# Kernel tuning notes

Hardware: AMD Instinct MI355X
Metric: run time of the kernel (lower is better)

The kernel has to match this reference:

```python
import jax, jax.numpy as jnp
import numpy as np

N = 80000       # nodes
E = 1280000     # edges (avg degree 16)
G = 2000        # graphs
NSHAPE, NCOLOR, POSMAX = 16, 16, 1024
HID, OUT, IN_DIM = 64, 2, 40
EPS = 1e-5


def setup_inputs() -> dict:
    key = jax.random.key(0)
    ks = jax.random.split(key, 20)
    f32 = jnp.float32
    return {
        "shape_id": jax.random.randint(ks[0], (N,), 0, NSHAPE),
        "color_id": jax.random.randint(ks[1], (N,), 0, NCOLOR),
        "pos_id": jax.random.randint(ks[2], (N,), 0, POSMAX),
        "edge_index": jax.random.randint(ks[3], (2, E), 0, N),
        "batch": jnp.sort(jax.random.randint(ks[4], (N,), 0, G)),
        "num_graphs": G,
        "shape_tab": jax.random.normal(ks[5], (NSHAPE, 16), f32),
        "color_tab": jax.random.normal(ks[6], (NCOLOR, 16), f32),
        "pos_tab": jax.random.normal(ks[7], (POSMAX, 8), f32),
        "W1l": jax.random.normal(ks[8], (IN_DIM, HID), f32) / np.sqrt(IN_DIM),
        "b1": jnp.zeros((HID,), f32),
        "W1r": jax.random.normal(ks[9], (IN_DIM, HID), f32) / np.sqrt(IN_DIM),
        "g1": jnp.ones((HID,), f32),
        "be1": jnp.zeros((HID,), f32),
        "W2l": jax.random.normal(ks[10], (HID, HID), f32) / np.sqrt(HID),
        "b2": jnp.zeros((HID,), f32),
        "W2r": jax.random.normal(ks[11], (HID, HID), f32) / np.sqrt(HID),
        "g2": jnp.ones((HID,), f32),
        "be2": jnp.zeros((HID,), f32),
        "Wout": jax.random.normal(ks[12], (HID, OUT), f32) / np.sqrt(HID),
        "bout": jnp.zeros((OUT,), f32),
    }


def sage_conv(x, src, dst, Wl, b, Wr, n_nodes):
    # PyG SAGEConv (mean aggr): out = lin_l(mean_{j in N(i)} x_j) + lin_r(x_i)
    agg = jax.ops.segment_sum(x[src], dst, num_segments=n_nodes)     # [N, F]
    deg = jax.ops.segment_sum(jnp.ones((src.shape[0], 1), x.dtype), dst,
                              num_segments=n_nodes)                  # [N, 1]
    agg = agg / jnp.maximum(deg, 1.0)
    return agg @ Wl + b + x @ Wr


def batch_norm(x, gamma, beta):
    # training-mode BatchNorm1d over nodes
    m = x.mean(axis=0)
    v = x.var(axis=0)
    return (x - m) * (gamma / jnp.sqrt(v + EPS)) + beta


def reference(shape_id, color_id, pos_id, edge_index, batch, num_graphs,
              shape_tab, color_tab, pos_tab,
              W1l, b1, W1r, g1, be1,
              W2l, b2, W2r, g2, be2,
              Wout, bout):
    n_nodes = shape_id.shape[0]
    src, dst = edge_index[0], edge_index[1]
    x = jnp.concatenate([shape_tab[shape_id], color_tab[color_id],
                         pos_tab[pos_id]], axis=-1)                  # [N, 40]
    x = jax.nn.relu(batch_norm(sage_conv(x, src, dst, W1l, b1, W1r, n_nodes), g1, be1))
    # dropout: eval mode -> identity
    x = jax.nn.relu(batch_norm(sage_conv(x, src, dst, W2l, b2, W2r, n_nodes), g2, be2))
    # global mean pool over batch segments
    summed = jax.ops.segment_sum(x, batch, num_segments=num_graphs)   # [G, H]
    counts = jax.ops.segment_sum(jnp.ones((n_nodes, 1), x.dtype), batch,
                                 num_segments=num_graphs)
    pooled = summed / jnp.maximum(counts, 1.0)
    return pooled @ Wout + bout                                       # [G, 2]
```

## Files before the change

### kernel.cpp

```cpp
#include <hip/hip_runtime.h>

#define NN 80000
#define NE 1280000
#define NG 2000
#define HID 64
#define FIN1 40
#define BSZ 128
#define NBUK (NN / BSZ)
#define EB 8192
#define NBB ((NE + EB - 1) / EB)
#define NBBP 160
constexpr float EPS = 1e-5f;

typedef _Float16 f16;
typedef f16 f16x8 __attribute__((ext_vector_type(8)));
typedef float f32x4 __attribute__((ext_vector_type(4)));

__global__ void setup(const int* __restrict__ sid, const int* __restrict__ cid,
                      const int* __restrict__ pid, const int* __restrict__ batch,
                      const float* __restrict__ stab, const float* __restrict__ ctab,
                      const float* __restrict__ ptab,
                      const float* __restrict__ W1l, const float* __restrict__ W1r,
                      const float* __restrict__ W2l, const float* __restrict__ W2r,
                      int* __restrict__ ids, f16* __restrict__ Bt1, f16* __restrict__ Bt2,
                      int* __restrict__ gstart,
                      f16* __restrict__ stab16, f16* __restrict__ ctab16,
                      f16* __restrict__ ptab16) {
    int bid = blockIdx.x;
    int tid = threadIdx.x;
    if (bid < 313) {
        int n = bid * 256 + tid;
        if (n < NN) ids[n] = sid[n] | (cid[n] << 4) | (pid[n] << 8);
    } else if (bid < 373) {
        int i = (bid - 313) * 256 + tid;
        if (i < 64 * 104) {
            int j = i / 104, k = i - j * 104;
            float v = 0.f;
            if (k < 40) v = W1l[k * 64 + j];
            else if (k < 80) v = W1r[(k - 40) * 64 + j];
            Bt1[i] = (f16)v;
        }
        int i2 = i - 64 * 104;
        if (i2 >= 0 && i2 < 64 * 136) {
            int j = i2 / 136, k = i2 - j * 136;
            float v = 0.f;
            if (k < 64) v = W2l[k * 64 + j];
            else if (k < 128) v = W2r[(k - 64) * 64 + j];
            Bt2[i2] = (f16)v;
        }
    } else if (bid < 686) {
        int n = (bid - 373) * 256 + tid;
        if (n >= NN) return;
        int cur = batch[n];
        int prev = (n == 0) ? -1 : batch[n - 1];
        for (int g = prev + 1; g <= cur; g++) gstart[g] = n;
        if (n == NN - 1)
            for (int g = cur + 1; g <= NG; g++) gstart[g] = NN;
    } else {
        int i = (bid - 686) * 256 + tid;
        if (i < 256) stab16[i] = (f16)stab[i];
        else if (i < 512) ctab16[i - 256] = (f16)ctab[i - 256];
        else if (i < 512 + 8192) ptab16[i - 512] = (f16)ptab[i - 512];
    }
}

__global__ void khist(const int* __restrict__ dst, int* __restrict__ bhistT,
                      int* __restrict__ bcnt) {
    __shared__ int lh[NBUK];
    for (int i = threadIdx.x; i < NBUK; i += 256) lh[i] = 0;
    __syncthreads();
    int e0 = blockIdx.x * EB, e1 = min(e0 + EB, NE);
    for (int e = e0 + threadIdx.x; e < e1; e += 256) atomicAdd(&lh[dst[e] >> 7], 1);
    __syncthreads();
    for (int i = threadIdx.x; i < NBUK; i += 256) {
        int c = lh[i];
        bhistT[i * NBBP + blockIdx.x] = c;
        if (c) atomicAdd(&bcnt[i], c);
    }
}

__global__ void kscan_a(const int* __restrict__ bcnt, int* __restrict__ bstart) {
    __shared__ int l[1024];
    int t = threadIdx.x;
    l[t] = (t < NBUK) ? bcnt[t] : 0;
    __syncthreads();
    for (int off = 1; off < 1024; off <<= 1) {
        int v = (t >= off) ? l[t - off] : 0;
        __syncthreads();
        l[t] += v;
        __syncthreads();
    }
    if (t < NBUK) bstart[t] = (t == 0) ? 0 : l[t - 1];
    if (t == NBUK) bstart[NBUK] = NE;
}

__global__ void kscan_b(const int* __restrict__ bhistT, const int* __restrict__ bstart,
                        int* __restrict__ lbaseT) {
    int b = blockIdx.x;
    int l = threadIdx.x;
    int run = bstart[b];
    for (int i0 = 0; i0 < NBB; i0 += 64) {
        int idx = i0 + l;
        int v = (idx < NBB) ? bhistT[b * NBBP + idx] : 0;
        int inc = v;
        for (int off = 1; off < 64; off <<= 1) {
            int tt = __shfl_up(inc, off);
            if (l >= off) inc += tt;
        }
        if (idx < NBB) lbaseT[b * NBBP + idx] = run + inc - v;
        run += __shfl(inc, 63);
    }
}

__global__ void kbin(const int* __restrict__ src, const int* __restrict__ dst,
                     const int* __restrict__ lbaseT, int* __restrict__ ebuf) {
    __shared__ int lcur[NBUK];
    for (int i = threadIdx.x; i < NBUK; i += 256) lcur[i] = lbaseT[i * NBBP + blockIdx.x];
    __syncthreads();
    int e0 = blockIdx.x * EB, e1 = min(e0 + EB, NE);
    for (int e = e0 + threadIdx.x; e < e1; e += 256) {
        int d = dst[e];
        int off = atomicAdd(&lcur[d >> 7], 1);
        ebuf[off] = (src[e] << 7) | (d & 127);
    }
}

__global__ void kfill(const int* __restrict__ ebuf, const int* __restrict__ bstart,
                      int* __restrict__ row_ptr, int* __restrict__ eidx) {
    __shared__ int cnt[BSZ];
    __shared__ int sb[BSZ];
    __shared__ int lcur[BSZ];
    int b = blockIdx.x, t = threadIdx.x;
    int nbase = b << 7;
    if (t < BSZ) cnt[t] = 0;
    __syncthreads();
    int s0 = bstart[b], s1 = bstart[b + 1];
    for (int i = s0 + t; i < s1; i += 256) atomicAdd(&cnt[ebuf[i] & 127], 1);
    __syncthreads();
    if (t < BSZ) sb[t] = cnt[t];
    __syncthreads();
    for (int off = 1; off < BSZ; off <<= 1) {
        int v = (t >= off && t < BSZ) ? sb[t - off] : 0;
        __syncthreads();
        if (t < BSZ) sb[t] += v;
        __syncthreads();
    }
    if (t < BSZ) {
        int excl = ((t == 0) ? 0 : sb[t - 1]) + s0;
        row_ptr[nbase + t] = excl;
        lcur[t] = excl;
    }
    if (b == 0 && t == 0) row_ptr[NN] = NE;
    __syncthreads();
    for (int i = s0 + t; i < s1; i += 256) {
        int v = ebuf[i];
        int pos = atomicAdd(&lcur[v & 127], 1);
        eidx[pos] = v >> 7;
    }
}

__global__ void gather1(const int* __restrict__ row_ptr, const int* __restrict__ eidx,
                        const int* __restrict__ ids,
                        const f16* __restrict__ stab16, const f16* __restrict__ ctab16,
                        const f16* __restrict__ ptab16, f16* __restrict__ agg) {
    int tt = blockIdx.x * 256 + threadIdx.x;
    int n = tt >> 6;
    int lane = threadIdx.x & 63;
    if (n >= NN) return;
    int grp = lane >> 3, li = lane & 7;
    int beg = row_ptr[n], end = row_ptr[n + 1];
    float ac[8];
#pragma unroll
    for (int i = 0; i < 8; i++) ac[i] = 0.f;
    for (int j0 = beg; j0 < end; j0 += 64) {
        int cnt = min(64, end - j0);
        int myid = (j0 + lane < end) ? eidx[j0 + lane] : 0;
        int steps = (cnt + 7) >> 3;
        for (int u = 0; u < steps; u++) {
            int e = u * 8 + grp;
            int s = __shfl(myid, e);
            if (e < cnt && li < 5) {
                int id = ids[s];
                const f16* rowp;
                if (li < 2)      rowp = &stab16[(id & 15) * 16 + li * 8];
                else if (li < 4) rowp = &ctab16[((id >> 4) & 15) * 16 + (li - 2) * 8];
                else             rowp = &ptab16[(id >> 8) * 8];
                f16x8 v = *(const f16x8*)rowp;
#pragma unroll
                for (int i = 0; i < 8; i++) ac[i] += (float)v[i];
            }
        }
    }
#pragma unroll
    for (int m = 8; m <= 32; m <<= 1) {
#pragma unroll
        for (int i = 0; i < 8; i++) ac[i] += __shfl_xor(ac[i], m);
    }
    if (lane < 5) {
        float inv = 1.0f / (float)max(end - beg, 1);
        f16x8 o;
#pragma unroll
        for (int i = 0; i < 8; i++) o[i] = (f16)(ac[i] * inv);
        *(f16x8*)&agg[(size_t)n * FIN1 + lane * 8] = o;
    }
}

__global__ void gather2(const int* __restrict__ row_ptr, const int* __restrict__ eidx,
                        const f16* __restrict__ x, const float* __restrict__ stats,
                        const float* __restrict__ g1, const float* __restrict__ be1,
                        f16* __restrict__ agg) {
    int tt = blockIdx.x * 256 + threadIdx.x;
    int n = tt >> 6;
    int lane = threadIdx.x & 63;
    if (n >= NN) return;
    int grp = lane >> 3;
    int fl = (lane & 7) * 8;
    float sc8[8], sh8[8];
    {
        const float invn = 1.0f / (float)NN;
#pragma unroll
        for (int i = 0; i < 8; i++) {
            float m = stats[fl + i] * invn;
            float var = stats[64 + fl + i] * invn - m * m;
            float sc = g1[fl + i] * __frsqrt_rn(var + EPS);
            sc8[i] = sc;
            sh8[i] = be1[fl + i] - m * sc;
        }
    }
    int beg = row_ptr[n], end = row_ptr[n + 1];
    float ac[8];
#pragma unroll
    for (int i = 0; i < 8; i++) ac[i] = 0.f;
    for (int j0 = beg; j0 < end; j0 += 64) {
        int cnt = min(64, end - j0);
        int myid = (j0 + lane < end) ? eidx[j0 + lane] : 0;
        int steps = (cnt + 7) >> 3;
        for (int u = 0; u < steps; u++) {
            int e = u * 8 + grp;
            int s = __shfl(myid, e);
            if (e < cnt) {
                f16x8 v = *(const f16x8*)&x[(size_t)s * HID + fl];
#pragma unroll
                for (int i = 0; i < 8; i++)
                    ac[i] += fmaxf(fmaf((float)v[i], sc8[i], sh8[i]), 0.f);
            }
        }
    }
#pragma unroll
    for (int m = 8; m <= 32; m <<= 1) {
#pragma unroll
        for (int i = 0; i < 8; i++) ac[i] += __shfl_xor(ac[i], m);
    }
    if (lane < 8) {
        float inv = 1.0f / (float)max(end - beg, 1);
        f16x8 o;
#pragma unroll
        for (int i = 0; i < 8; i++) o[i] = (f16)(ac[i] * inv);
        *(f16x8*)&agg[(size_t)n * HID + fl] = o;
    }
}

__launch_bounds__(256)
__global__ void sage_mfma1(const int* __restrict__ ids, const f16* __restrict__ aggv,
                           const f16* __restrict__ stab16, const f16* __restrict__ ctab16,
                           const f16* __restrict__ ptab16,
                           const f16* __restrict__ Btg, const float* __restrict__ bias,
                           f16* __restrict__ h, float* __restrict__ stats) {
    __shared__ float sred[4][64];
    __shared__ float qred[4][64];
    const int KP = 104;

    int tid = threadIdx.x;
    int n0 = blockIdx.x * 64;
    int w = tid >> 6, l = tid & 63;
    int jloc = l & 15, kg = l >> 4;
    int n = n0 + w * 16 + jloc;

    f16x8 af[3];
#pragma unroll
    for (int kk = 0; kk < 3; kk++) {
        int c = kk * 4 + kg;
        if (c < 5) {
            af[kk] = *(const f16x8*)&aggv[(size_t)n * FIN1 + c * 8];
        } else if (c < 10) {
            int id = ids[n];
            int cc = c - 5;
            const f16* rowp;
            if (cc < 2)      rowp = &stab16[(id & 15) * 16 + cc * 8];
            else if (cc < 4) rowp = &ctab16[((id >> 4) & 15) * 16 + (cc - 2) * 8];
            else             rowp = &ptab16[(id >> 8) * 8];
            af[kk] = *(const f16x8*)rowp;
        } else {
#pragma unroll
            for (int i = 0; i < 8; i++) af[kk][i] = (f16)0.f;
        }
    }

    f32x4 acc[4];
#pragma unroll
    for (int jt = 0; jt < 4; jt++) {
        float bj = bias[jt * 16 + jloc];
        acc[jt] = (f32x4){bj, bj, bj, bj};
    }
#pragma unroll
    for (int kk = 0; kk < 3; kk++) {
#pragma unroll
        for (int jt = 0; jt < 4; jt++) {
            f16x8 bf = *(const f16x8*)&Btg[(jt * 16 + jloc) * KP + kk * 32 + kg * 8];
            acc[jt] = __builtin_amdgcn_mfma_f32_16x16x32_f16(af[kk], bf, acc[jt], 0, 0, 0);
        }
    }
#pragma unroll
    for (int jt = 0; jt < 4; jt++) {
        float sv = 0.f, qv = 0.f;
#pragma unroll
        for (int reg = 0; reg < 4; reg++) {
            f16 hv = (f16)acc[jt][reg];
            int nn2 = n0 + w * 16 + kg * 4 + reg;
            h[(size_t)nn2 * HID + jt * 16 + jloc] = hv;
            float v = (float)hv;
            sv += v; qv += v * v;
        }
        sv += __shfl_xor(sv, 16); sv += __shfl_xor(sv, 32);
        qv += __shfl_xor(qv, 16); qv += __shfl_xor(qv, 32);
        if (kg == 0) { sred[w][jt * 16 + jloc] = sv; qred[w][jt * 16 + jloc] = qv; }
    }
    __syncthreads();
    if (tid < 128) {
        int f2 = tid & 63, which = tid >> 6;
        float r = which ? (qred[0][f2] + qred[1][f2] + qred[2][f2] + qred[3][f2])
                        : (sred[0][f2] + sred[1][f2] + sred[2][f2] + sred[3][f2]);
        atomicAdd(&stats[which * 64 + f2], r);
    }
}

__launch_bounds__(256)
__global__ void sage_mfma2(const f16* __restrict__ x, const f16* __restrict__ aggv,
                           const f16* __restrict__ Btg, const float* __restrict__ bias,
                           f16* __restrict__ h,
                           const float* __restrict__ stats1, const float* __restrict__ g1,
                           const float* __restrict__ be1, float* __restrict__ stats) {
    __shared__ float ssc[64], ssh[64];
    __shared__ float sred[4][64];
    __shared__ float qred[4][64];
    const int KP = 136;

    int tid = threadIdx.x;
    int n0 = blockIdx.x * 64;
    if (tid < 64) {
        const float invn = 1.0f / (float)NN;
        float m = stats1[tid] * invn;
        float var = stats1[64 + tid] * invn - m * m;
        float sc = g1[tid] * __frsqrt_rn(var + EPS);
        ssc[tid] = sc;
        ssh[tid] = be1[tid] - m * sc;
    }
    __syncthreads();

    int w = tid >> 6, l = tid & 63;
    int jloc = l & 15, kg = l >> 4;
    int n = n0 + w * 16 + jloc;

    f16x8 af[4];
#pragma unroll
    for (int kk = 0; kk < 4; kk++) {
        int c = kk * 4 + kg;
        if (c < 8) {
            af[kk] = *(const f16x8*)&aggv[(size_t)n * HID + c * 8];
        } else {
            int fb = (c - 8) * 8;
            f16x8 vx = *(const f16x8*)&x[(size_t)n * HID + fb];
#pragma unroll
            for (int i = 0; i < 8; i++)
                af[kk][i] = (f16)fmaxf(fmaf((float)vx[i], ssc[fb + i], ssh[fb + i]), 0.f);
        }
    }

    f32x4 acc[4];
#pragma unroll
    for (int jt = 0; jt < 4; jt++) {
        float bj = bias[jt * 16 + jloc];
        acc[jt] = (f32x4){bj, bj, bj, bj};
    }
#pragma unroll
    for (int kk = 0; kk < 4; kk++) {
#pragma unroll
        for (int jt = 0; jt < 4; jt++) {
            f16x8 bf = *(const f16x8*)&Btg[(jt * 16 + jloc) * KP + kk * 32 + kg * 8];
            acc[jt] = __builtin_amdgcn_mfma_f32_16x16x32_f16(af[kk], bf, acc[jt], 0, 0, 0);
        }
    }
#pragma unroll
    for (int jt = 0; jt < 4; jt++) {
        float sv = 0.f, qv = 0.f;
#pragma unroll
        for (int reg = 0; reg < 4; reg++) {
            f16 hv = (f16)acc[jt][reg];
            int nn2 = n0 + w * 16 + kg * 4 + reg;
            h[(size_t)nn2 * HID + jt * 16 + jloc] = hv;
            float v = (float)hv;
            sv += v; qv += v * v;
        }
        sv += __shfl_xor(sv, 16); sv += __shfl_xor(sv, 32);
        qv += __shfl_xor(qv, 16); qv += __shfl_xor(qv, 32);
        if (kg == 0) { sred[w][jt * 16 + jloc] = sv; qred[w][jt * 16 + jloc] = qv; }
    }
    __syncthreads();
    if (tid < 128) {
        int f2 = tid & 63, which = tid >> 6;
        float r = which ? (qred[0][f2] + qred[1][f2] + qred[2][f2] + qred[3][f2])
                        : (sred[0][f2] + sred[1][f2] + sred[2][f2] + sred[3][f2]);
        atomicAdd(&stats[which * 64 + f2], r);
    }
}

__global__ void pool_out(const f16* __restrict__ h, const float* __restrict__ stats2,
                         const float* __restrict__ g2, const float* __restrict__ be2,
                         const int* __restrict__ gstart,
                         const float* __restrict__ Wout, const float* __restrict__ bout,
                         float* __restrict__ out) {
    int w = (blockIdx.x * blockDim.x + threadIdx.x) >> 6;
    int f = threadIdx.x & 63;
    if (w >= NG) return;
    const float invn = 1.0f / (float)NN;
    float m = stats2[f] * invn;
    float var = stats2[64 + f] * invn - m * m;
    float sc = g2[f] / sqrtf(var + EPS);
    float sh = be2[f] - m * sc;
    int n0 = gstart[w], n1 = gstart[w + 1];
    float acc = 0.f;
    for (int n = n0; n < n1; n++) {
        float v = fmaf((float)h[(size_t)n * HID + f], sc, sh);
        acc += fmaxf(v, 0.0f);
    }
    float inv = 1.0f / (float)max(n1 - n0, 1);
    float p = acc * inv;
    float a0 = p * Wout[f * 2 + 0];
    float a1 = p * Wout[f * 2 + 1];
#pragma unroll
    for (int mm = 1; mm < 64; mm <<= 1) {
        a0 += __shfl_xor(a0, mm);
        a1 += __shfl_xor(a1, mm);
    }
    if (f == 0) {
        out[w * 2 + 0] = a0 + bout[0];
        out[w * 2 + 1] = a1 + bout[1];
    }
}

extern "C" void kernel_launch(void* const* d_in, const int* in_sizes, int n_in,
                              void* d_out, int out_size, void* d_ws, size_t ws_size,
                              hipStream_t stream) {
    const int* sid = (const int*)d_in[0];
    const int* cid = (const int*)d_in[1];
    const int* pid = (const int*)d_in[2];
    const int* ei = (const int*)d_in[3];
    const int* batch = (const int*)d_in[4];
    const float* stab = (const float*)d_in[6];
    const float* ctab = (const float*)d_in[7];
    const float* ptab = (const float*)d_in[8];
    const float* W1l = (const float*)d_in[9];
    const float* b1 = (const float*)d_in[10];
    const float* W1r = (const float*)d_in[11];
    const float* g1 = (const float*)d_in[12];
    const float* be1 = (const float*)d_in[13];
    const float* W2l = (const float*)d_in[14];
    const float* b2 = (const float*)d_in[15];
    const float* W2r = (const float*)d_in[16];
    const float* g2 = (const float*)d_in[17];
    const float* be2 = (const float*)d_in[18];
    const float* Wout = (const float*)d_in[19];
    const float* bout = (const float*)d_in[20];

    const int* src = ei;
    const int* dst = ei + NE;

    char* p = (char*)d_ws;
    f16* agg = (f16*)p;        p += (size_t)NN * HID * 2;
    f16* h1 = (f16*)p;         p += (size_t)NN * HID * 2;
    f16* h2 = (f16*)p;         p += (size_t)NN * HID * 2;
    f16* bt1 = (f16*)p;        p += 64 * 104 * 2;
    f16* bt2 = (f16*)p;        p += 64 * 136 * 2;
    f16* stab16 = (f16*)p;     p += 256 * 2;
    f16* ctab16 = (f16*)p;     p += 256 * 2;
    f16* ptab16 = (f16*)p;     p += 8192 * 2;
    float* stats = (float*)p;  p += 256 * 4;
    int* bcnt = (int*)p;       p += NBUK * 4;
    int* ids = (int*)p;        p += (size_t)NN * 4;
    int* row_ptr = (int*)p;    p += (NN + 1) * 4;
    int* gstart = (int*)p;     p += (NG + 1) * 4;
    int* bstart = (int*)p;     p += (NBUK + 1) * 4;
    int* bhistT = (int*)p;     p += (size_t)NBUK * NBBP * 4;
    int* lbaseT = (int*)p;     p += (size_t)NBUK * NBBP * 4;
    int* ebuf = (int*)p;       p += (size_t)NE * 4;
    int* eidx = (int*)p;       p += (size_t)NE * 4;

    hipMemsetAsync(stats, 0, 256 * 4 + NBUK * 4, stream);

    const int B = 256;

    setup<<<720, B, 0, stream>>>(sid, cid, pid, batch, stab, ctab, ptab,
                                 W1l, W1r, W2l, W2r,
                                 ids, bt1, bt2, gstart, stab16, ctab16, ptab16);

    khist<<<NBB, B, 0, stream>>>(dst, bhistT, bcnt);
    kscan_a<<<1, 1024, 0, stream>>>(bcnt, bstart);
    kscan_b<<<NBUK, 64, 0, stream>>>(bhistT, bstart, lbaseT);
    kbin<<<NBB, B, 0, stream>>>(src, dst, lbaseT, ebuf);
    kfill<<<NBUK, B, 0, stream>>>(ebuf, bstart, row_ptr, eidx);

    gather1<<<(NN * 64 + B - 1) / B, B, 0, stream>>>(row_ptr, eidx, ids,
                                                     stab16, ctab16, ptab16, agg);
    sage_mfma1<<<NN / 64, B, 0, stream>>>(ids, agg, stab16, ctab16, ptab16,
                                          bt1, b1, h1, stats);

    gather2<<<(NN * 64 + B - 1) / B, B, 0, stream>>>(row_ptr, eidx, h1, stats, g1, be1, agg);
    sage_mfma2<<<NN / 64, B, 0, stream>>>(h1, agg, bt2, b2, h2,
                                          stats, g1, be1, stats + 128);

    pool_out<<<(NG * 64 + B - 1) / B, B, 0, stream>>>(h2, stats + 128, g2, be2, gstart,
                                                      Wout, bout, (float*)d_out);
}
```

Baseline: 234.1 us.

## Repack gather1 lanes 12x5, batch gather loads, fold memset into setup

gather1 now assigns lanes as 12 edge groups times 5 feature slices, so 60 of 64 lanes do useful work where the old 8x8 layout used only 5 of every 8. It issues the eidx, ids and table loads for 5 edges up front to expose memory-level parallelism, and reduces across groups with custom shuffles. gather2 likewise hoists all 8 per-chunk loads before accumulating. The hipMemsetAsync of stats and bcnt is replaced by an extra setup block that zeroes them, which removes one launch. The unrolled loads raise register pressure, and the irregular shuffle reduction adds instructions.

```diff
diff --git a/kernel.cpp b/kernel.cpp
--- a/kernel.cpp
+++ b/kernel.cpp
@@ -25,7 +25,8 @@
                       int* __restrict__ ids, f16* __restrict__ Bt1, f16* __restrict__ Bt2,
                       int* __restrict__ gstart,
                       f16* __restrict__ stab16, f16* __restrict__ ctab16,
-                      f16* __restrict__ ptab16) {
+                      f16* __restrict__ ptab16,
+                      float* __restrict__ stats, int* __restrict__ bcnt) {
     int bid = blockIdx.x;
     int tid = threadIdx.x;
     if (bid < 313) {
@@ -56,11 +57,14 @@
         for (int g = prev + 1; g <= cur; g++) gstart[g] = n;
         if (n == NN - 1)
             for (int g = cur + 1; g <= NG; g++) gstart[g] = NN;
-    } else {
+    } else if (bid < 720) {
         int i = (bid - 686) * 256 + tid;
         if (i < 256) stab16[i] = (f16)stab[i];
         else if (i < 512) ctab16[i - 256] = (f16)ctab[i - 256];
         else if (i < 512 + 8192) ptab16[i - 512] = (f16)ptab[i - 512];
+    } else {
+        if (tid < 256) stats[tid] = 0.f;
+        for (int i = tid; i < NBUK; i += 256) bcnt[i] = 0;
     }
 }
 
@@ -167,34 +171,53 @@
     int n = tt >> 6;
     int lane = threadIdx.x & 63;
     if (n >= NN) return;
-    int grp = lane >> 3, li = lane & 7;
+    int grp = lane / 5;
+    int li = lane - grp * 5;
+    bool lact = grp < 12;
     int beg = row_ptr[n], end = row_ptr[n + 1];
     float ac[8];
 #pragma unroll
     for (int i = 0; i < 8; i++) ac[i] = 0.f;
-    for (int j0 = beg; j0 < end; j0 += 64) {
-        int cnt = min(64, end - j0);
-        int myid = (j0 + lane < end) ? eidx[j0 + lane] : 0;
-        int steps = (cnt + 7) >> 3;
-        for (int u = 0; u < steps; u++) {
-            int e = u * 8 + grp;
-            int s = __shfl(myid, e);
-            if (e < cnt && li < 5) {
-                int id = ids[s];
+    for (int j0 = beg; j0 < end; j0 += 60) {
+        int cnt = min(60, end - j0);
+        bool val[5];
+        int sidx[5];
+#pragma unroll
+        for (int u = 0; u < 5; u++) {
+            int e = u * 12 + grp;
+            val[u] = lact && (e < cnt);
+            sidx[u] = val[u] ? eidx[j0 + e] : 0;
+        }
+        int idv[5];
+#pragma unroll
+        for (int u = 0; u < 5; u++) idv[u] = val[u] ? ids[sidx[u]] : 0;
+        f16x8 v[5];
+#pragma unroll
+        for (int u = 0; u < 5; u++) {
+            if (val[u]) {
+                int id = idv[u];
                 const f16* rowp;
                 if (li < 2)      rowp = &stab16[(id & 15) * 16 + li * 8];
                 else if (li < 4) rowp = &ctab16[((id >> 4) & 15) * 16 + (li - 2) * 8];
                 else             rowp = &ptab16[(id >> 8) * 8];
-                f16x8 v = *(const f16x8*)rowp;
-#pragma unroll
-                for (int i = 0; i < 8; i++) ac[i] += (float)v[i];
+                v[u] = *(const f16x8*)rowp;
             }
         }
-    }
-#pragma unroll
-    for (int m = 8; m <= 32; m <<= 1) {
-#pragma unroll
-        for (int i = 0; i < 8; i++) ac[i] += __shfl_xor(ac[i], m);
+#pragma unroll
+        for (int u = 0; u < 5; u++) {
+            if (val[u]) {
+#pragma unroll
+                for (int i = 0; i < 8; i++) ac[i] += (float)v[u][i];
+            }
+        }
+    }
+#pragma unroll
+    for (int i = 0; i < 8; i++) {
+        float r;
+        r = __shfl(ac[i], lane + 30); if (grp < 6) ac[i] += r;
+        r = __shfl(ac[i], lane + 15); if (grp < 3) ac[i] += r;
+        r = __shfl(ac[i], lane + 10); if (grp < 1) ac[i] += r;
+        r = __shfl(ac[i], lane + 5);  if (grp < 1) ac[i] += r;
     }
     if (lane < 5) {
         float inv = 1.0f / (float)max(end - beg, 1);
@@ -233,16 +256,21 @@
     for (int i = 0; i < 8; i++) ac[i] = 0.f;
     for (int j0 = beg; j0 < end; j0 += 64) {
         int cnt = min(64, end - j0);
-        int myid = (j0 + lane < end) ? eidx[j0 + lane] : 0;
-        int steps = (cnt + 7) >> 3;
-        for (int u = 0; u < steps; u++) {
+        bool val[8];
+        f16x8 v[8];
+#pragma unroll
+        for (int u = 0; u < 8; u++) {
             int e = u * 8 + grp;
-            int s = __shfl(myid, e);
-            if (e < cnt) {
-                f16x8 v = *(const f16x8*)&x[(size_t)s * HID + fl];
+            val[u] = e < cnt;
+            int s = val[u] ? eidx[j0 + e] : 0;
+            if (val[u]) v[u] = *(const f16x8*)&x[(size_t)s * HID + fl];
+        }
+#pragma unroll
+        for (int u = 0; u < 8; u++) {
+            if (val[u]) {
 #pragma unroll
                 for (int i = 0; i < 8; i++)
-                    ac[i] += fmaxf(fmaf((float)v[i], sc8[i], sh8[i]), 0.f);
+                    ac[i] += fmaxf(fmaf((float)v[u][i], sc8[i], sh8[i]), 0.f);
             }
         }
     }
@@ -495,13 +523,12 @@
     int* ebuf = (int*)p;       p += (size_t)NE * 4;
     int* eidx = (int*)p;       p += (size_t)NE * 4;
 
-    hipMemsetAsync(stats, 0, 256 * 4 + NBUK * 4, stream);
-
     const int B = 256;
 
-    setup<<<720, B, 0, stream>>>(sid, cid, pid, batch, stab, ctab, ptab,
+    setup<<<721, B, 0, stream>>>(sid, cid, pid, batch, stab, ctab, ptab,
                                  W1l, W1r, W2l, W2r,
-                                 ids, bt1, bt2, gstart, stab16, ctab16, ptab16);
+                                 ids, bt1, bt2, gstart, stab16, ctab16, ptab16,
+                                 stats, bcnt);
 
     khist<<<NBB, B, 0, stream>>>(dst, bhistT, bcnt);
     kscan_a<<<1, 1024, 0, stream>>>(bcnt, bstart);
```

Result: slower. 250.5 us (+7.0%).

## Hoist layer-1 BN+ReLU into separate pass, accumulate gathers in fp16

Applied to the files above, without the earlier changes.

Adds a bn_apply16 kernel that applies batch-norm and ReLU to h1 once per node in place, so gather2 and sage_mfma2 read normalized values instead of recomputing the affine+ReLU per edge. Both gather kernels now accumulate neighbor features in packed fp16 vectors rather than fp32. The hipMemsetAsync is folded into an extra block of the setup kernel. The changes cut per-edge ALU work and one launch, at the cost of an extra pass over h1 and lower accumulation precision over up to dozens of neighbors.

```diff
diff --git a/kernel.cpp b/kernel.cpp
--- a/kernel.cpp
+++ b/kernel.cpp
@@ -25,7 +25,8 @@
                       int* __restrict__ ids, f16* __restrict__ Bt1, f16* __restrict__ Bt2,
                       int* __restrict__ gstart,
                       f16* __restrict__ stab16, f16* __restrict__ ctab16,
-                      f16* __restrict__ ptab16) {
+                      f16* __restrict__ ptab16,
+                      float* __restrict__ stats, int* __restrict__ bcnt) {
     int bid = blockIdx.x;
     int tid = threadIdx.x;
     if (bid < 313) {
@@ -56,11 +57,14 @@
         for (int g = prev + 1; g <= cur; g++) gstart[g] = n;
         if (n == NN - 1)
             for (int g = cur + 1; g <= NG; g++) gstart[g] = NN;
-    } else {
+    } else if (bid < 720) {
         int i = (bid - 686) * 256 + tid;
         if (i < 256) stab16[i] = (f16)stab[i];
         else if (i < 512) ctab16[i - 256] = (f16)ctab[i - 256];
         else if (i < 512 + 8192) ptab16[i - 512] = (f16)ptab[i - 512];
+    } else {
+        if (tid < 256) stats[tid] = 0.f;
+        for (int i = tid; i < NBUK; i += 256) bcnt[i] = 0;
     }
 }
 
@@ -168,10 +172,11 @@
     int lane = threadIdx.x & 63;
     if (n >= NN) return;
     int grp = lane >> 3, li = lane & 7;
+    bool act = li < 5;
     int beg = row_ptr[n], end = row_ptr[n + 1];
-    float ac[8];
-#pragma unroll
-    for (int i = 0; i < 8; i++) ac[i] = 0.f;
+    f16x8 ach;
+#pragma unroll
+    for (int i = 0; i < 8; i++) ach[i] = (f16)0.f;
     for (int j0 = beg; j0 < end; j0 += 64) {
         int cnt = min(64, end - j0);
         int myid = (j0 + lane < end) ? eidx[j0 + lane] : 0;
@@ -179,18 +184,19 @@
         for (int u = 0; u < steps; u++) {
             int e = u * 8 + grp;
             int s = __shfl(myid, e);
-            if (e < cnt && li < 5) {
+            if (e < cnt && act) {
                 int id = ids[s];
                 const f16* rowp;
                 if (li < 2)      rowp = &stab16[(id & 15) * 16 + li * 8];
                 else if (li < 4) rowp = &ctab16[((id >> 4) & 15) * 16 + (li - 2) * 8];
                 else             rowp = &ptab16[(id >> 8) * 8];
-                f16x8 v = *(const f16x8*)rowp;
-#pragma unroll
-                for (int i = 0; i < 8; i++) ac[i] += (float)v[i];
+                ach += *(const f16x8*)rowp;
             }
         }
     }
+    float ac[8];
+#pragma unroll
+    for (int i = 0; i < 8; i++) ac[i] = (float)ach[i];
 #pragma unroll
     for (int m = 8; m <= 32; m <<= 1) {
 #pragma unroll
@@ -205,32 +211,44 @@
     }
 }
 
+__global__ void bn_apply16(f16* __restrict__ h, const float* __restrict__ stats,
+                           const float* __restrict__ g, const float* __restrict__ be) {
+    __shared__ float ssc[64], ssh[64];
+    int tid = threadIdx.x;
+    if (tid < 64) {
+        const float invn = 1.0f / (float)NN;
+        float m = stats[tid] * invn;
+        float var = stats[64 + tid] * invn - m * m;
+        float sc = g[tid] * __frsqrt_rn(var + EPS);
+        ssc[tid] = sc;
+        ssh[tid] = be[tid] - m * sc;
+    }
+    __syncthreads();
+    int idx = blockIdx.x * 256 + tid;
+    if (idx >= NN * 8) return;
+    int f = (idx & 7) * 8;
+    f16x8 v = *(f16x8*)&h[(size_t)idx * 8];
+    f16x8 o;
+#pragma unroll
+    for (int i = 0; i < 8; i++) {
+        float xv = (float)v[i];
+        o[i] = (f16)fmaxf(fmaf(xv, ssc[f + i], ssh[f + i]), 0.f);
+    }
+    *(f16x8*)&h[(size_t)idx * 8] = o;
+}
+
 __global__ void gather2(const int* __restrict__ row_ptr, const int* __restrict__ eidx,
-                        const f16* __restrict__ x, const float* __restrict__ stats,
-                        const float* __restrict__ g1, const float* __restrict__ be1,
-                        f16* __restrict__ agg) {
+                        const f16* __restrict__ x, f16* __restrict__ agg) {
     int tt = blockIdx.x * 256 + threadIdx.x;
     int n = tt >> 6;
     int lane = threadIdx.x & 63;
     if (n >= NN) return;
     int grp = lane >> 3;
     int fl = (lane & 7) * 8;
-    float sc8[8], sh8[8];
-    {
-        const float invn = 1.0f / (float)NN;
-#pragma unroll
-        for (int i = 0; i < 8; i++) {
-            float m = stats[fl + i] * invn;
-            float var = stats[64 + fl + i] * invn - m * m;
-            float sc = g1[fl + i] * __frsqrt_rn(var + EPS);
-            sc8[i] = sc;
-            sh8[i] = be1[fl + i] - m * sc;
-        }
-    }
     int beg = row_ptr[n], end = row_ptr[n + 1];
-    float ac[8];
-#pragma unroll
-    for (int i = 0; i < 8; i++) ac[i] = 0.f;
+    f16x8 ach;
+#pragma unroll
+    for (int i = 0; i < 8; i++) ach[i] = (f16)0.f;
     for (int j0 = beg; j0 < end; j0 += 64) {
         int cnt = min(64, end - j0);
         int myid = (j0 + lane < end) ? eidx[j0 + lane] : 0;
@@ -239,13 +257,13 @@
             int e = u * 8 + grp;
             int s = __shfl(myid, e);
             if (e < cnt) {
-                f16x8 v = *(const f16x8*)&x[(size_t)s * HID + fl];
-#pragma unroll
-                for (int i = 0; i < 8; i++)
-                    ac[i] += fmaxf(fmaf((float)v[i], sc8[i], sh8[i]), 0.f);
+                ach += *(const f16x8*)&x[(size_t)s * HID + fl];
             }
         }
     }
+    float ac[8];
+#pragma unroll
+    for (int i = 0; i < 8; i++) ac[i] = (float)ach[i];
 #pragma unroll
     for (int m = 8; m <= 32; m <<= 1) {
 #pragma unroll
@@ -337,26 +355,13 @@
 __launch_bounds__(256)
 __global__ void sage_mfma2(const f16* __restrict__ x, const f16* __restrict__ aggv,
                            const f16* __restrict__ Btg, const float* __restrict__ bias,
-                           f16* __restrict__ h,
-                           const float* __restrict__ stats1, const float* __restrict__ g1,
-                           const float* __restrict__ be1, float* __restrict__ stats) {
-    __shared__ float ssc[64], ssh[64];
+                           f16* __restrict__ h, float* __restrict__ stats) {
     __shared__ float sred[4][64];
     __shared__ float qred[4][64];
     const int KP = 136;
 
     int tid = threadIdx.x;
     int n0 = blockIdx.x * 64;
-    if (tid < 64) {
-        const float invn = 1.0f / (float)NN;
-        float m = stats1[tid] * invn;
-        float var = stats1[64 + tid] * invn - m * m;
-        float sc = g1[tid] * __frsqrt_rn(var + EPS);
-        ssc[tid] = sc;
-        ssh[tid] = be1[tid] - m * sc;
-    }
-    __syncthreads();
-
     int w = tid >> 6, l = tid & 63;
     int jloc = l & 15, kg = l >> 4;
     int n = n0 + w * 16 + jloc;
@@ -365,15 +370,8 @@
 #pragma unroll
     for (int kk = 0; kk < 4; kk++) {
         int c = kk * 4 + kg;
-        if (c < 8) {
-            af[kk] = *(const f16x8*)&aggv[(size_t)n * HID + c * 8];
-        } else {
-            int fb = (c - 8) * 8;
-            f16x8 vx = *(const f16x8*)&x[(size_t)n * HID + fb];
-#pragma unroll
-            for (int i = 0; i < 8; i++)
-                af[kk][i] = (f16)fmaxf(fmaf((float)vx[i], ssc[fb + i], ssh[fb + i]), 0.f);
-        }
+        if (c < 8) af[kk] = *(const f16x8*)&aggv[(size_t)n * HID + c * 8];
+        else       af[kk] = *(const f16x8*)&x[(size_t)n * HID + (c - 8) * 8];
     }
 
     f32x4 acc[4];
@@ -495,13 +493,12 @@
     int* ebuf = (int*)p;       p += (size_t)NE * 4;
     int* eidx = (int*)p;       p += (size_t)NE * 4;
 
-    hipMemsetAsync(stats, 0, 256 * 4 + NBUK * 4, stream);
-
     const int B = 256;
 
-    setup<<<720, B, 0, stream>>>(sid, cid, pid, batch, stab, ctab, ptab,
+    setup<<<721, B, 0, stream>>>(sid, cid, pid, batch, stab, ctab, ptab,
                                  W1l, W1r, W2l, W2r,
-                                 ids, bt1, bt2, gstart, stab16, ctab16, ptab16);
+                                 ids, bt1, bt2, gstart, stab16, ctab16, ptab16,
+                                 stats, bcnt);
 
     khist<<<NBB, B, 0, stream>>>(dst, bhistT, bcnt);
     kscan_a<<<1, 1024, 0, stream>>>(bcnt, bstart);
@@ -513,10 +510,10 @@
                                                      stab16, ctab16, ptab16, agg);
     sage_mfma1<<<NN / 64, B, 0, stream>>>(ids, agg, stab16, ctab16, ptab16,
                                           bt1, b1, h1, stats);
-
-    gather2<<<(NN * 64 + B - 1) / B, B, 0, stream>>>(row_ptr, eidx, h1, stats, g1, be1, agg);
-    sage_mfma2<<<NN / 64, B, 0, stream>>>(h1, agg, bt2, b2, h2,
-                                          stats, g1, be1, stats + 128);
+    bn_apply16<<<(NN * 8 + B - 1) / B, B, 0, stream>>>(h1, stats, g1, be1);
+
+    gather2<<<(NN * 64 + B - 1) / B, B, 0, stream>>>(row_ptr, eidx, h1, agg);
+    sage_mfma2<<<NN / 64, B, 0, stream>>>(h1, agg, bt2, b2, h2, stats + 128);
 
     pool_out<<<(NG * 64 + B - 1) / B, B, 0, stream>>>(h2, stats + 128, g2, be2, gstart,
                                                       Wout, bout, (float*)d_out);
```

New measurement: 228.1 us. 2.6% less time.
